# Kernel tuning notes

Hardware: AMD Instinct MI355X
Metric: run time of the kernel (lower is better)

## Reference

```python
import jax, jax.numpy as jnp
from jax import lax
import numpy as np

TEMPERATURE = 0.8
TOP_K = 50
TOP_P = 0.9
REP_PENALTY = 1.2


def setup_inputs() -> dict:
    key = jax.random.key(0)
    k1, k2 = jax.random.split(key)
    B, V, T = 256, 50257, 2048
    logits = jax.random.normal(k1, (B, V), dtype=jnp.float32) * 4.0  # spread so top-p is non-trivial
    generated = jax.random.randint(k2, (B, T), 0, V, dtype=jnp.int64)
    return {"logits": logits, "generated": generated}


def reference(logits, generated):
    """One decode-step of LLM.generate: temperature -> repetition penalty ->
    top-k filter -> top-p (nucleus) filter -> softmax -> multinomial sample.
    Returns (next_token [B], probs [B, V])."""
    B, V = logits.shape
    x = logits / TEMPERATURE

    # repetition penalty: divide logits at every previously-generated token id
    rows = jnp.arange(B)[:, None]
    present = jnp.zeros((B, V), dtype=bool).at[rows, generated].set(True)
    x = jnp.where(present, x / REP_PENALTY, x)

    # top-k: mask everything strictly below the k-th largest logit
    kth = lax.top_k(x, TOP_K)[0][:, -1:]  # [B, 1]
    x = jnp.where(x < kth, -jnp.inf, x)

    # top-p: sort descending, softmax, cumsum, drop tail mass > p (always keep top-1)
    order = jnp.argsort(-x, axis=-1)                      # [B, V] descending order
    sorted_logits = jnp.take_along_axis(x, order, axis=-1)
    cum = jnp.cumsum(jax.nn.softmax(sorted_logits, axis=-1), axis=-1)
    remove_sorted = (cum > TOP_P).at[:, 0].set(False)
    inv = jnp.argsort(order, axis=-1)                     # inverse permutation
    remove = jnp.take_along_axis(remove_sorted, inv, axis=-1)
    x = jnp.where(remove, -jnp.inf, x)

    probs = jax.nn.softmax(x, axis=-1)
    # multinomial sampling == categorical over the filtered logits
    next_token = jax.random.categorical(jax.random.key(42), x, axis=-1)  # [B]
    return next_token, probs
```

## Files before the change

### kernel.cpp

```cpp
#include <hip/hip_runtime.h>
#include <stdint.h>

#define V_CONST 50257
#define NMASK ((V_CONST + 31) / 32)
#define KTOP 50
#define CAND_CAP 1024
#define NTHREADS 1024
#define C_TEMP 1.25f
#define C_PEN ((float)(1.25 / 1.2))
#define THREEFRY_PARTITIONABLE 1

__device__ __forceinline__ void tf_round(uint32_t &x0, uint32_t &x1, int r) {
  x0 += x1;
  x1 = (x1 << r) | (x1 >> (32 - r));
  x1 ^= x0;
}

__device__ __forceinline__ uint2 threefry_k_0_42(uint32_t x0, uint32_t x1) {
  const uint32_t ks0 = 0u;
  const uint32_t ks1 = 42u;
  const uint32_t ks2 = 0x1BD11BDAu ^ 0u ^ 42u;
  x0 += ks0; x1 += ks1;
  tf_round(x0, x1, 13); tf_round(x0, x1, 15); tf_round(x0, x1, 26); tf_round(x0, x1, 6);
  x0 += ks1; x1 += ks2 + 1u;
  tf_round(x0, x1, 17); tf_round(x0, x1, 29); tf_round(x0, x1, 16); tf_round(x0, x1, 24);
  x0 += ks2; x1 += ks0 + 2u;
  tf_round(x0, x1, 13); tf_round(x0, x1, 15); tf_round(x0, x1, 26); tf_round(x0, x1, 6);
  x0 += ks0; x1 += ks1 + 3u;
  tf_round(x0, x1, 17); tf_round(x0, x1, 29); tf_round(x0, x1, 16); tf_round(x0, x1, 24);
  x0 += ks1; x1 += ks2 + 4u;
  tf_round(x0, x1, 13); tf_round(x0, x1, 15); tf_round(x0, x1, 26); tf_round(x0, x1, 6);
  x0 += ks2; x1 += ks0 + 5u;
  uint2 r; r.x = x0; r.y = x1; return r;
}

__device__ __forceinline__ float gumbel_at(uint32_t p, uint32_t half_total) {
  uint32_t bits;
#if THREEFRY_PARTITIONABLE
  uint2 o = threefry_k_0_42(0u, p);
  bits = o.x ^ o.y;
#else
  if (p < half_total) {
    uint2 o = threefry_k_0_42(p, p + half_total);
    bits = o.x;
  } else {
    uint2 o = threefry_k_0_42(p - half_total, p);
    bits = o.y;
  }
#endif
  uint32_t ub = (bits >> 9) | 0x3F800000u;
  float u = __uint_as_float(ub) - 1.0f;
  u = u + 1.17549435e-38f;
  u = fmaxf(1.17549435e-38f, u);
  return -logf(-logf(u));
}

__device__ __forceinline__ uint32_t f2u_desc(float f) {
  uint32_t b = __float_as_uint(f);
  return (b & 0x80000000u) ? ~b : (b | 0x80000000u);
}
__device__ __forceinline__ float u2f(uint32_t u) {
  uint32_t b = (u & 0x80000000u) ? (u & 0x7FFFFFFFu) : ~u;
  return __uint_as_float(b);
}

__global__ __launch_bounds__(NTHREADS) void sample_kernel(
    const float* __restrict__ logits, const int* __restrict__ generated,
    float* __restrict__ out, int B, int T) {
  const int b = blockIdx.x;
  const int tid = threadIdx.x;

  __shared__ uint32_t mask[NMASK];
  __shared__ uint32_t candA[CAND_CAP];
  __shared__ int      cidx[CAND_CAP];
  __shared__ uint32_t su[CAND_CAP];
  __shared__ int      sidx[CAND_CAP];
  __shared__ float    eg[CAND_CAP];
  __shared__ float    gg[CAND_CAP];
  __shared__ int s_ncand, s_nsurv, s_rlast;
  __shared__ float s_z2;

  {
    size_t e0 = (size_t)B + (size_t)b * V_CONST;
    size_t e1 = e0 + V_CONST;
    size_t a0 = (e0 + 3) & ~(size_t)3;
    size_t a1 = e1 & ~(size_t)3;
    for (size_t e = e0 + tid; e < a0; e += NTHREADS) out[e] = 0.f;
    float4* o4 = (float4*)(out + a0);
    size_t n4 = (a1 - a0) >> 2;
    float4 z4 = make_float4(0.f, 0.f, 0.f, 0.f);
    for (size_t i = tid; i < n4; i += NTHREADS) o4[i] = z4;
    for (size_t e = a1 + tid; e < e1; e += NTHREADS) out[e] = 0.f;
  }

  for (int i = tid; i < NMASK; i += NTHREADS) mask[i] = 0u;
  __syncthreads();
  const int* grow = generated + (size_t)b * T;
  for (int i = tid; i < T; i += NTHREADS) {
    int tok = grow[i];
    atomicOr(&mask[tok >> 5], 1u << (tok & 31));
  }
  __syncthreads();

  const float* lrow = logits + (size_t)b * V_CONST;
  const int aoff = (4 - (b & 3)) & 3;
  const int tailn = (V_CONST - aoff) & 3;
  const int body4 = (V_CONST - aoff) >> 2;
  const float4* arow4 = (const float4*)(lrow + aoff);

  float thr = 13.0f;
  uint32_t ulo = 0u, uhi = 0xFFFFFFFFu;
  int n = 0;

  for (int attempt = 0; attempt < 64; ++attempt) {
    __syncthreads();
    if (tid == 0) s_ncand = 0;
    __syncthreads();

    for (int q = tid; q < body4; q += NTHREADS) {
      float4 r = arow4[q];
      int v0 = aoff + (q << 2);
      uint32_t w = (mask[v0 >> 5] >> (v0 & 31)) & 0xFu;
      float m0 = (w & 1u) ? C_PEN : C_TEMP;
      float m1 = (w & 2u) ? C_PEN : C_TEMP;
      float m2 = (w & 4u) ? C_PEN : C_TEMP;
      float m3 = (w & 8u) ? C_PEN : C_TEMP;
      if (r.x * m0 >= thr) { int p = atomicAdd(&s_ncand, 1); if (p < CAND_CAP) { candA[p] = __float_as_uint(r.x); cidx[p] = v0; } }
      if (r.y * m1 >= thr) { int p = atomicAdd(&s_ncand, 1); if (p < CAND_CAP) { candA[p] = __float_as_uint(r.y); cidx[p] = v0 + 1; } }
      if (r.z * m2 >= thr) { int p = atomicAdd(&s_ncand, 1); if (p < CAND_CAP) { candA[p] = __float_as_uint(r.z); cidx[p] = v0 + 2; } }
      if (r.w * m3 >= thr) { int p = atomicAdd(&s_ncand, 1); if (p < CAND_CAP) { candA[p] = __float_as_uint(r.w); cidx[p] = v0 + 3; } }
    }
    if (tid < aoff + tailn) {
      int v = (tid < aoff) ? tid : (V_CONST - tailn) + (tid - aoff);
      float x = lrow[v];
      float m = ((mask[v >> 5] >> (v & 31)) & 1u) ? C_PEN : C_TEMP;
      if (x * m >= thr) { int p = atomicAdd(&s_ncand, 1); if (p < CAND_CAP) { candA[p] = __float_as_uint(x); cidx[p] = v; } }
    }
    __syncthreads();

    const int total = s_ncand;
    n = (total < CAND_CAP) ? total : CAND_CAP;
    const bool window = (total >= KTOP && total <= CAND_CAP);
    const bool last = (attempt == 63);

    if (window || last) {
      if (n > 0) {
        for (int i = tid; i < n; i += NTHREADS) {
          float x = __uint_as_float(candA[i]);
          int v = cidx[i];
          float xe = x / 0.8f;
          if ((mask[v >> 5] >> (v & 31)) & 1u) xe = xe / 1.2f;
          candA[i] = f2u_desc(xe);
        }
        __syncthreads();
        for (int i = tid; i < n; i += NTHREADS) {
          uint32_t ui = candA[i]; int ii = cidx[i];
          int rank = 0;
          for (int j = 0; j < n; j++) {
            uint32_t uj = candA[j];
            rank += ((uj > ui) || (uj == ui && cidx[j] < ii)) ? 1 : 0;
          }
          su[rank] = ui; sidx[rank] = ii;
        }
        __syncthreads();
      }
      if (window) {
        uint32_t ut = f2u_desc(thr);
        if (su[KTOP - 1] >= ut + 64u) break;
        if (last) break;
        thr = u2f(su[KTOP - 1] >= 96u ? su[KTOP - 1] - 96u : 0u);
      } else {
        break;
      }
    } else if (total < KTOP) {
      uhi = f2u_desc(thr);
      if (attempt == 0) thr = 11.0f;
      else {
        uint32_t mid = ulo + (uhi - ulo) / 2u;
        if (mid >= uhi) mid = uhi - 1u;
        thr = u2f(mid);
      }
    } else {
      ulo = f2u_desc(thr);
      uint32_t mid = ulo + (uhi - ulo) / 2u;
      if (mid <= ulo) mid = ulo + 1u;
      thr = u2f(mid);
    }
  }

  if (n == 0) {
    if (tid == 0) out[b] = 0.f;
    return;
  }

  if (tid == 0) {
    int kpos = (n < KTOP) ? (n - 1) : (KTOP - 1);
    uint32_t kth = su[kpos];
    int ns = kpos + 1;
    while (ns < n && su[ns] == kth) ns++;
    s_nsurv = ns;
  }
  __syncthreads();
  const int nsurv = s_nsurv;
  const float s0 = u2f(su[0]);
  const uint32_t half_total = (uint32_t)((size_t)256 * V_CONST / 2);

  for (int r = tid; r < nsurv; r += NTHREADS) {
    float f = u2f(su[r]);
    eg[r] = expf(f - s0);
    gg[r] = gumbel_at((uint32_t)(b * V_CONST + sidx[r]), half_total);
  }
  __syncthreads();

  if (tid == 0) {
    float zall = 0.f;
    for (int r = 0; r < nsurv; r++) zall += eg[r];
    float cum = 0.f;
    int rlast = 0;
    for (int r = 0; r < nsurv; r++) {
      cum += eg[r] / zall;
      if (r == 0 || cum <= 0.9f) rlast = r;
      else break;
    }
    float z2 = 0.f;
    for (int r = 0; r <= rlast; r++) z2 += eg[r];
    float best = -3.402823466e38f; int besti = V_CONST;
    for (int r = 0; r <= rlast; r++) {
      float sc = u2f(su[r]) + gg[r];
      int idx = sidx[r];
      if (sc > best || (sc == best && idx < besti)) { best = sc; besti = idx; }
    }
    out[b] = (float)besti;
    s_rlast = rlast; s_z2 = z2;
  }
  __syncthreads();
  const int rlast = s_rlast;
  const float z2 = s_z2;

  {
    float* prow = out + B + (size_t)b * V_CONST;
    for (int r = tid; r <= rlast; r += NTHREADS) {
      prow[sidx[r]] = eg[r] / z2;
    }
  }
}

extern "C" void kernel_launch(void* const* d_in, const int* in_sizes, int n_in,
                              void* d_out, int out_size, void* d_ws, size_t ws_size,
                              hipStream_t stream) {
  const float* logits = (const float*)d_in[0];
  const int* generated = (const int*)d_in[1];
  float* out = (float*)d_out;
  const int B = in_sizes[0] / V_CONST;
  const int T = in_sizes[1] / B;
  hipLaunchKernelGGL(sample_kernel, dim3(B), dim3(NTHREADS), 0, stream,
                     logits, generated, out, B, T);
}
```

Measured before the change: 33.98 us.

## Split sampling into quarter-row screening kernel and per-row selection kernel

Moves the full-vocabulary scan, output zeroing and repetition-mask build into a first kernel that runs four blocks per row, each covering a quarter of the vocabulary and writing the candidates that pass a fixed threshold to workspace. A second kernel with one block per row gathers those candidates, ranks them and samples, and keeps the old adaptive threshold search only as a fallback when the fast path fails. The aim is more parallelism across the GPU and a smaller per-row critical path. The cost is an extra launch, a workspace round trip, and each row's generated tokens being read four times.

```diff
diff --git a/kernel.cpp b/kernel.cpp
--- a/kernel.cpp
+++ b/kernel.cpp
@@ -4,10 +4,15 @@
 #define V_CONST 50257
 #define NMASK ((V_CONST + 31) / 32)
 #define KTOP 50
-#define CAND_CAP 1024
-#define NTHREADS 1024
+#define NQ 4
+#define Q4 12565
+#define CAP_Q 512
+#define CAND_CAP 2048
+#define THR_SCREEN 13.0f
 #define C_TEMP 1.25f
 #define C_PEN ((float)(1.25 / 1.2))
+#define K1_THREADS 256
+#define K2_THREADS 256
 #define THREEFRY_PARTITIONABLE 1
 
 __device__ __forceinline__ void tf_round(uint32_t &x0, uint32_t &x1, int r) {
@@ -64,134 +69,226 @@
   return __uint_as_float(b);
 }
 
-__global__ __launch_bounds__(NTHREADS) void sample_kernel(
+__global__ __launch_bounds__(K1_THREADS) void screen_kernel(
     const float* __restrict__ logits, const int* __restrict__ generated,
-    float* __restrict__ out, int B, int T) {
+    float* __restrict__ out, uint2* __restrict__ pairs, int* __restrict__ counts,
+    int B, int T) {
+  const int bid = blockIdx.x;
+  const int row = bid >> 2, q = bid & 3;
+  const int tid = threadIdx.x;
+  const int vlo = q * Q4;
+  const int vhi = min(V_CONST, vlo + Q4);
+  const int len = vhi - vlo;
+  const int w0 = vlo >> 5;
+  const int nw = ((vhi + 31) >> 5) - w0;
+
+  __shared__ uint32_t qmask[(Q4 >> 5) + 2];
+  __shared__ int s_cnt;
+
+  for (int i = tid; i < nw; i += K1_THREADS) qmask[i] = 0u;
+  if (tid == 0) s_cnt = 0;
+  __syncthreads();
+
+  const int* grow = generated + (size_t)row * T;
+  for (int i = tid; i < T; i += K1_THREADS) {
+    int tok = grow[i];
+    if (tok >= vlo && tok < vhi)
+      atomicOr(&qmask[(tok >> 5) - w0], 1u << (tok & 31));
+  }
+  __syncthreads();
+
+  {
+    size_t e0 = (size_t)B + (size_t)row * V_CONST + vlo;
+    size_t e1 = e0 + len;
+    size_t a0 = (e0 + 3) & ~(size_t)3;
+    size_t a1 = e1 & ~(size_t)3;
+    for (size_t e = e0 + tid; e < a0; e += K1_THREADS) out[e] = 0.f;
+    float4* o4 = (float4*)(out + a0);
+    size_t n4 = (a1 - a0) >> 2;
+    float4 z4 = make_float4(0.f, 0.f, 0.f, 0.f);
+    for (size_t i = tid; i < n4; i += K1_THREADS) o4[i] = z4;
+    for (size_t e = a1 + tid; e < e1; e += K1_THREADS) out[e] = 0.f;
+  }
+
+  const float* lrow = logits + (size_t)row * V_CONST;
+  const int aoff = (4 - ((row + q) & 3)) & 3;
+  const int body4 = (len - aoff) >> 2;
+  const int tailn = (len - aoff) & 3;
+  const float4* arow4 = (const float4*)(lrow + vlo + aoff);
+  uint2* mypairs = pairs + (size_t)bid * CAP_Q;
+
+#define SCREEN1(xv, vv) do {                                          \
+    int v_ = (vv); float x_ = (xv);                                   \
+    uint32_t pres_ = (qmask[(v_ >> 5) - w0] >> (v_ & 31)) & 1u;       \
+    float m_ = pres_ ? C_PEN : C_TEMP;                                \
+    if (x_ * m_ >= THR_SCREEN) {                                      \
+      float xe_ = x_ / 0.8f; if (pres_) xe_ = xe_ / 1.2f;             \
+      int p_ = atomicAdd(&s_cnt, 1);                                  \
+      if (p_ < CAP_Q) mypairs[p_] = make_uint2(f2u_desc(xe_), (uint32_t)v_); \
+    } } while (0)
+
+  for (int t = tid; t < body4; t += K1_THREADS) {
+    float4 r = arow4[t];
+    int v0 = vlo + aoff + (t << 2);
+    SCREEN1(r.x, v0 + 0);
+    SCREEN1(r.y, v0 + 1);
+    SCREEN1(r.z, v0 + 2);
+    SCREEN1(r.w, v0 + 3);
+  }
+  if (tid < aoff + tailn) {
+    int v = (tid < aoff) ? (vlo + tid) : (vhi - tailn + (tid - aoff));
+    SCREEN1(lrow[v], v);
+  }
+#undef SCREEN1
+  __syncthreads();
+  if (tid == 0) counts[bid] = s_cnt;
+}
+
+__global__ __launch_bounds__(K2_THREADS) void sample_kernel2(
+    const float* __restrict__ logits, const int* __restrict__ generated,
+    float* __restrict__ out, const uint2* __restrict__ pairs,
+    const int* __restrict__ counts, int B, int T) {
   const int b = blockIdx.x;
   const int tid = threadIdx.x;
 
-  __shared__ uint32_t mask[NMASK];
-  __shared__ uint32_t candA[CAND_CAP];
+  __shared__ uint32_t cu[CAND_CAP];
   __shared__ int      cidx[CAND_CAP];
   __shared__ uint32_t su[CAND_CAP];
   __shared__ int      sidx[CAND_CAP];
   __shared__ float    eg[CAND_CAP];
   __shared__ float    gg[CAND_CAP];
+  __shared__ uint32_t mask[NMASK];
   __shared__ int s_ncand, s_nsurv, s_rlast;
   __shared__ float s_z2;
 
-  {
-    size_t e0 = (size_t)B + (size_t)b * V_CONST;
-    size_t e1 = e0 + V_CONST;
-    size_t a0 = (e0 + 3) & ~(size_t)3;
-    size_t a1 = e1 & ~(size_t)3;
-    for (size_t e = e0 + tid; e < a0; e += NTHREADS) out[e] = 0.f;
-    float4* o4 = (float4*)(out + a0);
-    size_t n4 = (a1 - a0) >> 2;
-    float4 z4 = make_float4(0.f, 0.f, 0.f, 0.f);
-    for (size_t i = tid; i < n4; i += NTHREADS) o4[i] = z4;
-    for (size_t e = a1 + tid; e < e1; e += NTHREADS) out[e] = 0.f;
-  }
-
-  for (int i = tid; i < NMASK; i += NTHREADS) mask[i] = 0u;
-  __syncthreads();
-  const int* grow = generated + (size_t)b * T;
-  for (int i = tid; i < T; i += NTHREADS) {
-    int tok = grow[i];
-    atomicOr(&mask[tok >> 5], 1u << (tok & 31));
-  }
-  __syncthreads();
-
-  const float* lrow = logits + (size_t)b * V_CONST;
-  const int aoff = (4 - (b & 3)) & 3;
-  const int tailn = (V_CONST - aoff) & 3;
-  const int body4 = (V_CONST - aoff) >> 2;
-  const float4* arow4 = (const float4*)(lrow + aoff);
-
-  float thr = 13.0f;
-  uint32_t ulo = 0u, uhi = 0xFFFFFFFFu;
+  int cq[NQ];
+  int total = 0;
+  bool ovf = false;
+  #pragma unroll
+  for (int q = 0; q < NQ; q++) {
+    cq[q] = counts[b * NQ + q];
+    if (cq[q] > CAP_Q) ovf = true;
+    total += cq[q];
+  }
+  bool fast = (!ovf) && total >= KTOP && total <= CAND_CAP;
   int n = 0;
-
-  for (int attempt = 0; attempt < 64; ++attempt) {
+  bool ok = false;
+
+  if (fast) {
+    int off = 0;
+    #pragma unroll
+    for (int q = 0; q < NQ; q++) {
+      const uint2* pp = pairs + (size_t)(b * NQ + q) * CAP_Q;
+      for (int i = tid; i < cq[q]; i += K2_THREADS) {
+        uint2 pr = pp[i];
+        cu[off + i] = pr.x; cidx[off + i] = (int)pr.y;
+      }
+      off += cq[q];
+    }
+    n = total;
     __syncthreads();
-    if (tid == 0) s_ncand = 0;
+    for (int i = tid; i < n; i += K2_THREADS) {
+      uint32_t ui = cu[i]; int ii = cidx[i];
+      int rank = 0;
+      for (int j = 0; j < n; j++) {
+        uint32_t uj = cu[j];
+        rank += ((uj > ui) || (uj == ui && cidx[j] < ii)) ? 1 : 0;
+      }
+      su[rank] = ui; sidx[rank] = ii;
+    }
     __syncthreads();
-
-    for (int q = tid; q < body4; q += NTHREADS) {
-      float4 r = arow4[q];
-      int v0 = aoff + (q << 2);
-      uint32_t w = (mask[v0 >> 5] >> (v0 & 31)) & 0xFu;
-      float m0 = (w & 1u) ? C_PEN : C_TEMP;
-      float m1 = (w & 2u) ? C_PEN : C_TEMP;
-      float m2 = (w & 4u) ? C_PEN : C_TEMP;
-      float m3 = (w & 8u) ? C_PEN : C_TEMP;
-      if (r.x * m0 >= thr) { int p = atomicAdd(&s_ncand, 1); if (p < CAND_CAP) { candA[p] = __float_as_uint(r.x); cidx[p] = v0; } }
-      if (r.y * m1 >= thr) { int p = atomicAdd(&s_ncand, 1); if (p < CAND_CAP) { candA[p] = __float_as_uint(r.y); cidx[p] = v0 + 1; } }
-      if (r.z * m2 >= thr) { int p = atomicAdd(&s_ncand, 1); if (p < CAND_CAP) { candA[p] = __float_as_uint(r.z); cidx[p] = v0 + 2; } }
-      if (r.w * m3 >= thr) { int p = atomicAdd(&s_ncand, 1); if (p < CAND_CAP) { candA[p] = __float_as_uint(r.w); cidx[p] = v0 + 3; } }
-    }
-    if (tid < aoff + tailn) {
-      int v = (tid < aoff) ? tid : (V_CONST - tailn) + (tid - aoff);
-      float x = lrow[v];
-      float m = ((mask[v >> 5] >> (v & 31)) & 1u) ? C_PEN : C_TEMP;
-      if (x * m >= thr) { int p = atomicAdd(&s_ncand, 1); if (p < CAND_CAP) { candA[p] = __float_as_uint(x); cidx[p] = v; } }
-    }
+    if (su[KTOP - 1] >= f2u_desc(THR_SCREEN) + 64u) ok = true;
+  }
+
+  if (!ok) {
+    for (int i = tid; i < NMASK; i += K2_THREADS) mask[i] = 0u;
     __syncthreads();
-
-    const int total = s_ncand;
-    n = (total < CAND_CAP) ? total : CAND_CAP;
-    const bool window = (total >= KTOP && total <= CAND_CAP);
-    const bool last = (attempt == 63);
-
-    if (window || last) {
-      if (n > 0) {
-        for (int i = tid; i < n; i += NTHREADS) {
-          float x = __uint_as_float(candA[i]);
-          int v = cidx[i];
-          float xe = x / 0.8f;
-          if ((mask[v >> 5] >> (v & 31)) & 1u) xe = xe / 1.2f;
-          candA[i] = f2u_desc(xe);
+    const int* grow = generated + (size_t)b * T;
+    for (int i = tid; i < T; i += K2_THREADS) {
+      int tok = grow[i];
+      atomicOr(&mask[tok >> 5], 1u << (tok & 31));
+    }
+    __syncthreads();
+    const float* lrow = logits + (size_t)b * V_CONST;
+    const int aoff = (4 - (b & 3)) & 3;
+    const int tailn = (V_CONST - aoff) & 3;
+    const int body4 = (V_CONST - aoff) >> 2;
+    const float4* arow4 = (const float4*)(lrow + aoff);
+    float thr = THR_SCREEN;
+    uint32_t ulo_ = 0u, uhi_ = 0xFFFFFFFFu;
+    n = 0;
+    for (int attempt = 0; attempt < 64; ++attempt) {
+      __syncthreads();
+      if (tid == 0) s_ncand = 0;
+      __syncthreads();
+      for (int t = tid; t < body4; t += K2_THREADS) {
+        float4 r = arow4[t];
+        int v0 = aoff + (t << 2);
+        uint32_t w = (mask[v0 >> 5] >> (v0 & 31)) & 0xFu;
+        float m0 = (w & 1u) ? C_PEN : C_TEMP;
+        float m1 = (w & 2u) ? C_PEN : C_TEMP;
+        float m2 = (w & 4u) ? C_PEN : C_TEMP;
+        float m3 = (w & 8u) ? C_PEN : C_TEMP;
+        if (r.x * m0 >= thr) { int p = atomicAdd(&s_ncand, 1); if (p < CAND_CAP) { cu[p] = __float_as_uint(r.x); cidx[p] = v0; } }
+        if (r.y * m1 >= thr) { int p = atomicAdd(&s_ncand, 1); if (p < CAND_CAP) { cu[p] = __float_as_uint(r.y); cidx[p] = v0 + 1; } }
+        if (r.z * m2 >= thr) { int p = atomicAdd(&s_ncand, 1); if (p < CAND_CAP) { cu[p] = __float_as_uint(r.z); cidx[p] = v0 + 2; } }
+        if (r.w * m3 >= thr) { int p = atomicAdd(&s_ncand, 1); if (p < CAND_CAP) { cu[p] = __float_as_uint(r.w); cidx[p] = v0 + 3; } }
+      }
+      if (tid < aoff + tailn) {
+        int v = (tid < aoff) ? tid : (V_CONST - tailn) + (tid - aoff);
+        float x = lrow[v];
+        float m = ((mask[v >> 5] >> (v & 31)) & 1u) ? C_PEN : C_TEMP;
+        if (x * m >= thr) { int p = atomicAdd(&s_ncand, 1); if (p < CAND_CAP) { cu[p] = __float_as_uint(x); cidx[p] = v; } }
+      }
+      __syncthreads();
+      const int tot = s_ncand;
+      n = (tot < CAND_CAP) ? tot : CAND_CAP;
+      const bool window = (tot >= KTOP && tot <= CAND_CAP);
+      const bool last = (attempt == 63);
+      if (window || last) {
+        if (n > 0) {
+          for (int i = tid; i < n; i += K2_THREADS) {
+            float x = __uint_as_float(cu[i]);
+            int v = cidx[i];
+            float xe = x / 0.8f;
+            if ((mask[v >> 5] >> (v & 31)) & 1u) xe = xe / 1.2f;
+            cu[i] = f2u_desc(xe);
+          }
+          __syncthreads();
+          for (int i = tid; i < n; i += K2_THREADS) {
+            uint32_t ui = cu[i]; int ii = cidx[i];
+            int rank = 0;
+            for (int j = 0; j < n; j++) {
+              uint32_t uj = cu[j];
+              rank += ((uj > ui) || (uj == ui && cidx[j] < ii)) ? 1 : 0;
+            }
+            su[rank] = ui; sidx[rank] = ii;
+          }
+          __syncthreads();
         }
-        __syncthreads();
-        for (int i = tid; i < n; i += NTHREADS) {
-          uint32_t ui = candA[i]; int ii = cidx[i];
-          int rank = 0;
-          for (int j = 0; j < n; j++) {
-            uint32_t uj = candA[j];
-            rank += ((uj > ui) || (uj == ui && cidx[j] < ii)) ? 1 : 0;
-          }
-          su[rank] = ui; sidx[rank] = ii;
+        if (window) {
+          if (su[KTOP - 1] >= f2u_desc(thr) + 64u) break;
+          if (last) break;
+          thr = u2f(su[KTOP - 1] >= 96u ? su[KTOP - 1] - 96u : 0u);
+        } else break;
+      } else if (tot < KTOP) {
+        uhi_ = f2u_desc(thr);
+        if (attempt == 0) thr = 11.0f;
+        else {
+          uint32_t mid = ulo_ + (uhi_ - ulo_) / 2u;
+          if (mid >= uhi_) mid = uhi_ - 1u;
+          thr = u2f(mid);
         }
-        __syncthreads();
-      }
-      if (window) {
-        uint32_t ut = f2u_desc(thr);
-        if (su[KTOP - 1] >= ut + 64u) break;
-        if (last) break;
-        thr = u2f(su[KTOP - 1] >= 96u ? su[KTOP - 1] - 96u : 0u);
       } else {
-        break;
-      }
-    } else if (total < KTOP) {
-      uhi = f2u_desc(thr);
-      if (attempt == 0) thr = 11.0f;
-      else {
-        uint32_t mid = ulo + (uhi - ulo) / 2u;
-        if (mid >= uhi) mid = uhi - 1u;
+        ulo_ = f2u_desc(thr);
+        uint32_t mid = ulo_ + (uhi_ - ulo_) / 2u;
+        if (mid <= ulo_) mid = ulo_ + 1u;
         thr = u2f(mid);
       }
-    } else {
-      ulo = f2u_desc(thr);
-      uint32_t mid = ulo + (uhi - ulo) / 2u;
-      if (mid <= ulo) mid = ulo + 1u;
-      thr = u2f(mid);
-    }
-  }
-
-  if (n == 0) {
-    if (tid == 0) out[b] = 0.f;
-    return;
-  }
+    }
+  }
+
+  if (n == 0) { if (tid == 0) out[b] = 0.f; return; }
 
   if (tid == 0) {
     int kpos = (n < KTOP) ? (n - 1) : (KTOP - 1);
@@ -205,7 +302,7 @@
   const float s0 = u2f(su[0]);
   const uint32_t half_total = (uint32_t)((size_t)256 * V_CONST / 2);
 
-  for (int r = tid; r < nsurv; r += NTHREADS) {
+  for (int r = tid; r < nsurv; r += K2_THREADS) {
     float f = u2f(su[r]);
     eg[r] = expf(f - s0);
     gg[r] = gumbel_at((uint32_t)(b * V_CONST + sidx[r]), half_total);
@@ -237,11 +334,9 @@
   const int rlast = s_rlast;
   const float z2 = s_z2;
 
-  {
-    float* prow = out + B + (size_t)b * V_CONST;
-    for (int r = tid; r <= rlast; r += NTHREADS) {
-      prow[sidx[r]] = eg[r] / z2;
-    }
+  float* prow = out + B + (size_t)b * V_CONST;
+  for (int r = tid; r <= rlast; r += K2_THREADS) {
+    prow[sidx[r]] = eg[r] / z2;
   }
 }
 
@@ -253,6 +348,10 @@
   float* out = (float*)d_out;
   const int B = in_sizes[0] / V_CONST;
   const int T = in_sizes[1] / B;
-  hipLaunchKernelGGL(sample_kernel, dim3(B), dim3(NTHREADS), 0, stream,
-                     logits, generated, out, B, T);
-}
+  int* counts = (int*)d_ws;
+  uint2* pairs = (uint2*)((char*)d_ws + 4096);
+  hipLaunchKernelGGL(screen_kernel, dim3(B * NQ), dim3(K1_THREADS), 0, stream,
+                     logits, generated, out, pairs, counts, B, T);
+  hipLaunchKernelGGL(sample_kernel2, dim3(B), dim3(K2_THREADS), 0, stream,
+                     logits, generated, out, pairs, counts, B, T);
+}
```

Result: slower. 73.07 us (+115.0%).
